# Kernel tuning notes

Measured on AMD Instinct MI355X. Metric: run time of the kernel, lower is better.

The kernel has to match this reference:

```python
import jax, jax.numpy as jnp
import numpy as np

N = 20000          # num nodes
DEG = 8            # directed avg degree before symmetrization
IN_C, HID, OUT_C, K = 128, 32, 16, 2


def _build_graph(n, deg, seed=0):
    """Build symmetric 1-hop A1 (no self loops) and exact 2-hop A2 edge lists,
    with D^{-1/2} A D^{-1/2} normalized values (mirrors _prepare_prop)."""
    rng = np.random.default_rng(seed)
    e = n * deg
    row = rng.integers(0, n, e)
    col = rng.integers(0, n, e)
    r = np.concatenate([row, col])
    c = np.concatenate([col, row])
    m = r != c
    keys1 = np.unique(r[m].astype(np.int64) * n + c[m])  # A1 = indicator(A - I)
    r1 = (keys1 // n).astype(np.int64)
    c1 = (keys1 % n).astype(np.int64)
    # exact 2-hop: nonzeros of A1@A1, minus A1 and diagonal
    degs = np.bincount(r1, minlength=n)
    indptr = np.concatenate([np.zeros(1, np.int64), np.cumsum(degs)])
    counts = degs[c1]                       # per edge (u,v): deg(v)
    cum = np.cumsum(counts)
    total = int(cum[-1])
    offs = np.arange(total) - np.repeat(cum - counts, counts)
    dst2 = c1[np.repeat(indptr[c1], counts) + offs]
    src2 = np.repeat(r1, counts)
    keys2 = np.unique(src2 * n + dst2)
    diag = np.arange(n, dtype=np.int64) * (n + 1)
    keys2 = np.setdiff1d(keys2, np.concatenate([keys1, diag]), assume_unique=True)
    r2 = (keys2 // n).astype(np.int64)
    c2 = (keys2 % n).astype(np.int64)

    def norm(rr, cc):  # D^{-1/2} A D^{-1/2} on binary symmetric adjacency
        d = np.bincount(rr, minlength=n).astype(np.float64)
        dis = np.where(d > 0, 1.0 / np.sqrt(np.maximum(d, 1.0)), 0.0)
        return (dis[rr] * dis[cc]).astype(np.float32)

    return r1, c1, norm(r1, c1), r2, c2, norm(r2, c2)


def setup_inputs() -> dict:
    key = jax.random.key(0)
    k1, k2, k3 = jax.random.split(key, 3)
    x = jax.random.normal(k1, (N, IN_C), dtype=jnp.float32)
    # xavier_uniform for the two dense weights
    ae = float(np.sqrt(6.0 / (IN_C + HID)))
    cdim = (2 ** (K + 1) - 1) * HID  # 224
    ac = float(np.sqrt(6.0 / (cdim + OUT_C)))
    w_embed = jax.random.uniform(k2, (IN_C, HID), jnp.float32, -ae, ae)
    w_classify = jax.random.uniform(k3, (cdim, OUT_C), jnp.float32, -ac, ac)
    r1, c1, v1, r2, c2, v2 = _build_graph(N, DEG)
    return {
        "x": x, "w_embed": w_embed, "w_classify": w_classify,
        "a1_row": jnp.asarray(r1), "a1_col": jnp.asarray(c1), "a1_val": jnp.asarray(v1),
        "a2_row": jnp.asarray(r2), "a2_col": jnp.asarray(c2), "a2_val": jnp.asarray(v2),
    }


def _spmm(row, col, val, x, n):
    # sparse @ dense: gather source rows, scale, scatter-add into dest rows
    return jax.ops.segment_sum(x[col] * val[:, None], row, num_segments=n)


def reference(x, w_embed, w_classify, a1_row, a1_col, a1_val, a2_row, a2_col, a2_val):
    n = x.shape[0]
    rs = [jax.nn.relu(x @ w_embed)]  # [N, HID]
    for _ in range(K):
        r = rs[-1]
        r1 = _spmm(a1_row, a1_col, a1_val, r, n)
        r2 = _spmm(a2_row, a2_col, a2_val, r, n)
        rs.append(jax.nn.relu(jnp.concatenate([r1, r2], axis=1)))
    r_final = jnp.concatenate(rs, axis=1)  # [N, 7*HID]; dropout is identity in eval
    return r_final @ w_classify            # [N, OUT_C]
```

## Files before the change

### kernel.cpp

```cpp
#include <hip/hip_runtime.h>

typedef unsigned int uint;
typedef unsigned short ushort;

#define IN_C 128
#define HID  32

__device__ __forceinline__ uint f2h2(float a, float b) {
    _Float16 ha = (_Float16)a, hb = (_Float16)b;
    unsigned short ua = __builtin_bit_cast(unsigned short, ha);
    unsigned short ub = __builtin_bit_cast(unsigned short, hb);
    return (uint)ua | ((uint)ub << 16);
}
__device__ __forceinline__ void fma_lo(float& acc, uint pk, float v) {
    asm("v_fma_mix_f32 %0, %1, %2, %0 op_sel:[0,0,0] op_sel_hi:[1,0,0]"
        : "+v"(acc) : "v"(pk), "v"(v));
}
__device__ __forceinline__ void fma_hi(float& acc, uint pk, float v) {
    asm("v_fma_mix_f32 %0, %1, %2, %0 op_sel:[1,0,0] op_sel_hi:[1,0,0]"
        : "+v"(acc) : "v"(pk), "v"(v));
}

__global__ void prep_kernel(const float* __restrict__ x,
                            const float* __restrict__ w,
                            ushort* __restrict__ r0,
                            const int* __restrict__ a1r, int E1, int* __restrict__ ip1,
                            const int* __restrict__ a2r, int E2, int* __restrict__ ip2,
                            const int* __restrict__ a2c, const float* __restrict__ a2v,
                            float* __restrict__ dummy,
                            int n, int nbE, int nbI, int nbT) {
    __shared__ float wl[IN_C * HID];
    const int tid = threadIdx.x;
    if (blockIdx.x < nbE) {
        for (int i = tid; i < IN_C * HID; i += blockDim.x) wl[i] = w[i];
        __syncthreads();
        const int row = blockIdx.x * 16 + tid / 16;
        const int h0  = (tid % 16) * 2;
        if (row >= n) return;
        const float4* xr = (const float4*)(x + (size_t)row * IN_C);
        float a0 = 0.f, a1 = 0.f;
#pragma unroll
        for (int k4 = 0; k4 < IN_C / 4; ++k4) {
            float4 xv = xr[k4];
            a0 += xv.x * wl[(4*k4+0)*HID + h0];  a1 += xv.x * wl[(4*k4+0)*HID + h0+1];
            a0 += xv.y * wl[(4*k4+1)*HID + h0];  a1 += xv.y * wl[(4*k4+1)*HID + h0+1];
            a0 += xv.z * wl[(4*k4+2)*HID + h0];  a1 += xv.z * wl[(4*k4+2)*HID + h0+1];
            a0 += xv.w * wl[(4*k4+3)*HID + h0];  a1 += xv.w * wl[(4*k4+3)*HID + h0+1];
        }
        uint p = f2h2(fmaxf(a0, 0.f), fmaxf(a1, 0.f));
        ((uint*)r0)[(size_t)row * 16 + (tid % 16)] = p;
    } else if (blockIdx.x < nbE + nbI) {
        const int i = (blockIdx.x - nbE) * 256 + tid;
        if (i > n) return;
        int lo = 0, hi = E1;
        while (lo < hi) { int m = (lo + hi) >> 1; if (a1r[m] < i) lo = m + 1; else hi = m; }
        ip1[i] = lo;
        lo = 0; hi = E2;
        while (lo < hi) { int m = (lo + hi) >> 1; if (a2r[m] < i) lo = m + 1; else hi = m; }
        ip2[i] = lo;
    } else {
        const int t = (blockIdx.x - nbE - nbI) * 256 + tid;
        const int stride = nbT * 256;
        const int total4 = E2 / 4;
        const float4* c4 = (const float4*)a2c;
        const float4* v4 = (const float4*)a2v;
        float s = 0.f;
        for (int i = t; i < total4; i += stride) {
            float4 u = c4[i], v = v4[i];
            s += u.x + u.y + u.z + u.w + v.x + v.y + v.z + v.w;
        }
        if (s == 123.456f) dummy[0] = s;
    }
}

template <int C, int ROWS>
__global__ __launch_bounds__(256) void spmm_level(
        const int* __restrict__ ip1, const int* __restrict__ col1,
        const float* __restrict__ val1,
        const int* __restrict__ ip2, const int* __restrict__ col2,
        const float* __restrict__ val2,
        const ushort* __restrict__ xin, ushort* __restrict__ out,
        int n, int nb2) {
    constexpr int L    = C / 8;
    constexpr int SUBL = 64 / ROWS;
    constexpr int W    = SUBL / L;
    const int lane = threadIdx.x & 63;
    const int wave = threadIdx.x >> 6;
    const int sub  = lane / SUBL;
    const int li   = lane % SUBL;
    const int fl   = li % L;
    const int way  = li / L;

    int bid = blockIdx.x;
    const int* ip; const int* col; const float* val; int off;
    if (bid < nb2) {             ip = ip2; col = col2; val = val2; off = C; }
    else           { bid -= nb2; ip = ip1; col = col1; val = val1; off = 0; }

    const int row = (bid * 4 + wave) * ROWS + sub;
    if (row >= n) return;

    const uint flo = (uint)fl * 16u;
    float acc[8];
#pragma unroll
    for (int j = 0; j < 8; ++j) acc[j] = 0.f;

    auto gat = [&](uint c) -> uint4 {
        return *(const uint4*)((const char*)xin + (c * (uint)(2 * C) + flo));
    };
    auto fmadd = [&](const uint4& u, float v) {
        fma_lo(acc[0], u.x, v); fma_hi(acc[1], u.x, v);
        fma_lo(acc[2], u.y, v); fma_hi(acc[3], u.y, v);
        fma_lo(acc[4], u.z, v); fma_hi(acc[5], u.z, v);
        fma_lo(acc[6], u.w, v); fma_hi(acc[7], u.w, v);
    };

    const int s = ip[row];
    const int e = ip[row + 1];
    int sv = (s + 3) & ~3; if (sv > e) sv = e;
    const int nv = (e - sv) / (4 * W);

    for (int idx = s + way; idx < sv; idx += W) fmadd(gat((uint)col[idx]), val[idx]);

    const int*   cb = col + sv;
    const float* vb = val + sv;
    for (int i = 0; i < nv; ++i) {
        const int base = (i * W + way) * 4;
        const int4   cc = *(const int4*)  (cb + base);
        const float4 vv = *(const float4*)(vb + base);
        const uint4 g0 = gat((uint)cc.x), g1 = gat((uint)cc.y),
                    g2 = gat((uint)cc.z), g3 = gat((uint)cc.w);
        fmadd(g0, vv.x); fmadd(g1, vv.y); fmadd(g2, vv.z); fmadd(g3, vv.w);
    }
    for (int idx = sv + nv * 4 * W + way; idx < e; idx += W)
        fmadd(gat((uint)col[idx]), val[idx]);

#pragma unroll
    for (int m = L; m < SUBL; m <<= 1)
#pragma unroll
        for (int j = 0; j < 8; ++j) acc[j] += __shfl_xor(acc[j], m, 64);

    if (way == 0) {
        uint4 p;
        p.x = f2h2(fmaxf(acc[0], 0.f), fmaxf(acc[1], 0.f));
        p.y = f2h2(fmaxf(acc[2], 0.f), fmaxf(acc[3], 0.f));
        p.z = f2h2(fmaxf(acc[4], 0.f), fmaxf(acc[5], 0.f));
        p.w = f2h2(fmaxf(acc[6], 0.f), fmaxf(acc[7], 0.f));
        *(uint4*)(out + (size_t)row * (2 * C) + off + fl * 8) = p;
    }
}

#define CDIM 224
#define OUT_C 16
__global__ void classify_kernel(const ushort* __restrict__ r0,
                                const ushort* __restrict__ r1,
                                const ushort* __restrict__ r2,
                                const float* __restrict__ w,
                                float* __restrict__ out, int n) {
    __shared__ float wl[CDIM * OUT_C];
    const int tid = threadIdx.x;
    for (int i = tid; i < CDIM * OUT_C; i += blockDim.x) wl[i] = w[i];
    __syncthreads();
    const int row = blockIdx.x * 16 + tid / 16;
    const int o   = tid % 16;
    if (row >= n) return;
    float acc = 0.f;

    const uint4* a = (const uint4*)(r0 + (size_t)row * 32);
#pragma unroll
    for (int q = 0; q < 4; ++q) {
        uint4 u = a[q]; int j = q * 8;
        fma_lo(acc, u.x, wl[(j+0)*OUT_C + o]);  fma_hi(acc, u.x, wl[(j+1)*OUT_C + o]);
        fma_lo(acc, u.y, wl[(j+2)*OUT_C + o]);  fma_hi(acc, u.y, wl[(j+3)*OUT_C + o]);
        fma_lo(acc, u.z, wl[(j+4)*OUT_C + o]);  fma_hi(acc, u.z, wl[(j+5)*OUT_C + o]);
        fma_lo(acc, u.w, wl[(j+6)*OUT_C + o]);  fma_hi(acc, u.w, wl[(j+7)*OUT_C + o]);
    }
    const uint4* b = (const uint4*)(r1 + (size_t)row * 64);
#pragma unroll
    for (int q = 0; q < 8; ++q) {
        uint4 u = b[q]; int j = 32 + q * 8;
        fma_lo(acc, u.x, wl[(j+0)*OUT_C + o]);  fma_hi(acc, u.x, wl[(j+1)*OUT_C + o]);
        fma_lo(acc, u.y, wl[(j+2)*OUT_C + o]);  fma_hi(acc, u.y, wl[(j+3)*OUT_C + o]);
        fma_lo(acc, u.z, wl[(j+4)*OUT_C + o]);  fma_hi(acc, u.z, wl[(j+5)*OUT_C + o]);
        fma_lo(acc, u.w, wl[(j+6)*OUT_C + o]);  fma_hi(acc, u.w, wl[(j+7)*OUT_C + o]);
    }
    const uint4* c = (const uint4*)(r2 + (size_t)row * 128);
#pragma unroll
    for (int q = 0; q < 16; ++q) {
        uint4 u = c[q]; int j = 96 + q * 8;
        fma_lo(acc, u.x, wl[(j+0)*OUT_C + o]);  fma_hi(acc, u.x, wl[(j+1)*OUT_C + o]);
        fma_lo(acc, u.y, wl[(j+2)*OUT_C + o]);  fma_hi(acc, u.y, wl[(j+3)*OUT_C + o]);
        fma_lo(acc, u.z, wl[(j+4)*OUT_C + o]);  fma_hi(acc, u.z, wl[(j+5)*OUT_C + o]);
        fma_lo(acc, u.w, wl[(j+6)*OUT_C + o]);  fma_hi(acc, u.w, wl[(j+7)*OUT_C + o]);
    }
    out[(size_t)row * OUT_C + o] = acc;
}

extern "C" void kernel_launch(void* const* d_in, const int* in_sizes, int n_in,
                              void* d_out, int out_size, void* d_ws, size_t ws_size,
                              hipStream_t stream) {
    const float* x   = (const float*)d_in[0];
    const float* we  = (const float*)d_in[1];
    const float* wc  = (const float*)d_in[2];
    const int*   a1r = (const int*)  d_in[3];
    const int*   a1c = (const int*)  d_in[4];
    const float* a1v = (const float*)d_in[5];
    const int*   a2r = (const int*)  d_in[6];
    const int*   a2c = (const int*)  d_in[7];
    const float* a2v = (const float*)d_in[8];
    float* out = (float*)d_out;

    const int E1 = in_sizes[3];
    const int E2 = in_sizes[6];
    const int n  = in_sizes[0] / IN_C;

    ushort* r0 = (ushort*)d_ws;
    ushort* r1 = r0 + (size_t)n * 32;
    ushort* r2 = r1 + (size_t)n * 64;
    int*   ip1 = (int*)(r2 + (size_t)n * 128);
    int*   ip2 = ip1 + (n + 1);
    float* dummy = (float*)(ip2 + (n + 2));

    {
        const int nbE = (n + 15) / 16;
        const int nbI = (n + 1 + 255) / 256;
        const int nbT = 512;
        prep_kernel<<<nbE + nbI + nbT, 256, 0, stream>>>(
            x, we, r0, a1r, E1, ip1, a2r, E2, ip2, a2c, a2v, dummy,
            n, nbE, nbI, nbT);
    }

    {
        const int nb = (n + 7) / 8;
        spmm_level<32, 2><<<2 * nb, 256, 0, stream>>>(ip1, a1c, a1v, ip2, a2c, a2v,
                                                      r0, r1, n, nb);
    }
    {
        const int nb = (n + 3) / 4;
        spmm_level<64, 1><<<2 * nb, 256, 0, stream>>>(ip1, a1c, a1v, ip2, a2c, a2v,
                                                      r1, r2, n, nb);
    }

    classify_kernel<<<(n + 15) / 16, 256, 0, stream>>>(r0, r1, r2, wc, out, n);
}
```

Before: 222.1 us.

## Software-pipeline gathers in SpMM with separate paths for 2-hop and 1-hop rows

Splits the per-row SpMM loop into a heavy path (2-hop adjacency) and a light path (1-hop adjacency). The heavy path prefetches column/value vectors two iterations ahead and feature gathers one iteration ahead. The light path runs a scalar loop that prefetches the next index and gather. The goal is to hide gather latency with more loads in flight, at the cost of extra registers, possible wasted clamped loads, and lower occupancy.

```diff
diff --git a/kernel.cpp b/kernel.cpp
--- a/kernel.cpp
+++ b/kernel.cpp
@@ -92,9 +92,9 @@
     const int way  = li / L;
 
     int bid = blockIdx.x;
-    const int* ip; const int* col; const float* val; int off;
-    if (bid < nb2) {             ip = ip2; col = col2; val = val2; off = C; }
-    else           { bid -= nb2; ip = ip1; col = col1; val = val1; off = 0; }
+    const int* ip; const int* col; const float* val; int off; bool heavy;
+    if (bid < nb2) {             ip = ip2; col = col2; val = val2; off = C; heavy = true;  }
+    else           { bid -= nb2; ip = ip1; col = col1; val = val1; off = 0; heavy = false; }
 
     const int row = (bid * 4 + wave) * ROWS + sub;
     if (row >= n) return;
@@ -116,23 +116,62 @@
 
     const int s = ip[row];
     const int e = ip[row + 1];
-    int sv = (s + 3) & ~3; if (sv > e) sv = e;
-    const int nv = (e - sv) / (4 * W);
-
-    for (int idx = s + way; idx < sv; idx += W) fmadd(gat((uint)col[idx]), val[idx]);
-
-    const int*   cb = col + sv;
-    const float* vb = val + sv;
-    for (int i = 0; i < nv; ++i) {
-        const int base = (i * W + way) * 4;
-        const int4   cc = *(const int4*)  (cb + base);
-        const float4 vv = *(const float4*)(vb + base);
-        const uint4 g0 = gat((uint)cc.x), g1 = gat((uint)cc.y),
-                    g2 = gat((uint)cc.z), g3 = gat((uint)cc.w);
-        fmadd(g0, vv.x); fmadd(g1, vv.y); fmadd(g2, vv.z); fmadd(g3, vv.w);
-    }
-    for (int idx = sv + nv * 4 * W + way; idx < e; idx += W)
-        fmadd(gat((uint)col[idx]), val[idx]);
+
+    if (heavy) {
+        int sv = (s + 3) & ~3; if (sv > e) sv = e;
+        const int nv = (e > sv) ? (e - sv) / (4 * W) : 0;
+
+        for (int idx = s + way; idx < sv; idx += W) fmadd(gat((uint)col[idx]), val[idx]);
+
+        const int*   cb = col + sv;
+        const float* vb = val + sv;
+        if (nv > 0) {
+            auto eboff = [&](int i) {
+                int ii = (i < nv) ? i : (nv - 1);
+                return (ii * W + way) * 4;
+            };
+            int b0 = eboff(0);
+            int4   cA = *(const int4*)  (cb + b0);
+            float4 vA = *(const float4*)(vb + b0);
+            int b1 = eboff(1);
+            int4   cB = *(const int4*)  (cb + b1);
+            float4 vB = *(const float4*)(vb + b1);
+            uint4 gA0 = gat((uint)cA.x), gA1 = gat((uint)cA.y),
+                  gA2 = gat((uint)cA.z), gA3 = gat((uint)cA.w);
+            for (int i = 0; i < nv; ++i) {
+                int b2 = eboff(i + 2);
+                int4   cC = *(const int4*)  (cb + b2);
+                float4 vC = *(const float4*)(vb + b2);
+                uint4 gB0 = gat((uint)cB.x), gB1 = gat((uint)cB.y),
+                      gB2 = gat((uint)cB.z), gB3 = gat((uint)cB.w);
+                fmadd(gA0, vA.x); fmadd(gA1, vA.y);
+                fmadd(gA2, vA.z); fmadd(gA3, vA.w);
+                gA0 = gB0; gA1 = gB1; gA2 = gB2; gA3 = gB3;
+                cB = cC; vA = vB; vB = vC;
+            }
+        }
+        for (int idx = sv + nv * 4 * W + way; idx < e; idx += W)
+            fmadd(gat((uint)col[idx]), val[idx]);
+    } else {
+        int idx0 = s + way;
+        if (idx0 < e) {
+            int c0 = col[idx0]; float v0 = val[idx0];
+            int idx1 = idx0 + W;
+            int c1 = 0; float v1 = 0.f;
+            if (idx1 < e) { c1 = col[idx1]; v1 = val[idx1]; }
+            uint4 g0 = gat((uint)c0);
+            while (true) {
+                int idx2 = idx1 + W;
+                int c2 = 0; float v2 = 0.f;
+                if (idx2 < e) { c2 = col[idx2]; v2 = val[idx2]; }
+                uint4 g1 = gat((uint)c1);
+                fmadd(g0, v0);
+                if (idx1 >= e) break;
+                g0 = g1; c1 = c2; v0 = v1; v1 = v2;
+                idx1 = idx2;
+            }
+        }
+    }
 
 #pragma unroll
     for (int m = L; m < SUBL; m <<= 1)
```

New measurement: 211.1 us. 5.0% less time.
